# Kernel tuning notes

Measured on AMD Instinct MI355X. Metric: run time of the kernel, lower is better.

The kernel has to match this reference:

```python
import jax, jax.numpy as jnp
import numpy as np

B, S, D, H, DK = 2, 2048, 1024, 16, 64  # d_model = n_heads * d_k

def setup_inputs() -> dict:
    key = jax.random.key(0)
    ks = jax.random.split(key, 11)
    s = 1.0 / np.sqrt(D)
    return {
        "Q": jax.random.normal(ks[0], (B, S, D), jnp.float32),
        "K": jax.random.normal(ks[1], (B, S, D), jnp.float32),
        "V": jax.random.normal(ks[2], (B, S, D), jnp.float32),
        "wq": jax.random.normal(ks[3], (D, D), jnp.float32) * s,
        "bq": jnp.zeros((D,), jnp.float32),
        "wk": jax.random.normal(ks[4], (D, D), jnp.float32) * s,
        "bk": jnp.zeros((D,), jnp.float32),
        "wv": jax.random.normal(ks[5], (D, D), jnp.float32) * s,
        "bv": jnp.zeros((D,), jnp.float32),
        "wo": jax.random.normal(ks[6], (D, D), jnp.float32) * s,
        "bo": jnp.zeros((D,), jnp.float32),
    }

def reference(Q, K, V, wq, bq, wk, bk, wv, bv, wo, bo):
    # linear projections (torch Linear: x @ W^T + b)
    q = Q @ wq.T + bq
    k = K @ wk.T + bk
    v = V @ wv.T + bv
    # split heads -> [B, H, S, DK]
    def split(t):
        return t.reshape(B, S, H, DK).transpose(0, 2, 1, 3)
    q, k, v = split(q), split(k), split(v)
    scale = 1.0 / np.sqrt(DK)
    scores = jnp.einsum('bhqd,bhkd->bhqk', q, k) * scale  # [B,H,S,S]
    probs = jax.nn.softmax(scores, axis=-1)
    # dropout is identity in eval mode
    ctx = jnp.einsum('bhqk,bhkd->bhqd', probs, v)  # [B,H,S,DK]
    ctx = ctx.transpose(0, 2, 1, 3).reshape(B, S, D)
    return ctx @ wo.T + bo
```

## Files before the change

kernel.cpp:

```cpp
#include <hip/hip_runtime.h>

#define S_LEN 2048
#define DMODEL 1024
#define DHEAD 64

typedef _Float16 half8 __attribute__((ext_vector_type(8)));
typedef _Float16 half4 __attribute__((ext_vector_type(4)));
typedef float f32x4 __attribute__((ext_vector_type(4)));
typedef int i32x4 __attribute__((ext_vector_type(4)));

#define LOG2E 1.4426950408889634f

__device__ __forceinline__ void async_copy16(const void* g, void* l) {
  __builtin_amdgcn_global_load_lds((__attribute__((address_space(1))) const void*)g,
                                   (__attribute__((address_space(3))) void*)l,
                                   16, 0, 0);
}

__global__ __launch_bounds__(256) void convert_w(const float* __restrict__ wq,
                                                 const float* __restrict__ wk,
                                                 const float* __restrict__ wv,
                                                 _Float16* __restrict__ dst) {
  const float* src = (blockIdx.y == 0) ? wq : (blockIdx.y == 1) ? wk : wv;
  _Float16* d = dst + (size_t)blockIdx.y * (DMODEL * DMODEL);
  int i = (blockIdx.x * 256 + threadIdx.x) * 4;
  float4 v = *(const float4*)(src + i);
  half4 h;
  h[0] = (_Float16)v.x; h[1] = (_Float16)v.y;
  h[2] = (_Float16)v.z; h[3] = (_Float16)v.w;
  *(half4*)(d + i) = h;
}

__global__ __launch_bounds__(256) void convert_wo(const float* __restrict__ wo,
                                                  _Float16* __restrict__ dst) {
  int i = (blockIdx.x * 256 + threadIdx.x) * 4;
  float4 v = *(const float4*)(wo + i);
  half4 h;
  h[0] = (_Float16)v.x; h[1] = (_Float16)v.y;
  h[2] = (_Float16)v.z; h[3] = (_Float16)v.w;
  *(half4*)(dst + i) = h;
}

__global__ __launch_bounds__(256) void qkv_gemm(
    const float* __restrict__ Qf, const float* __restrict__ Kf, const float* __restrict__ Vf,
    const _Float16* __restrict__ wh,
    const float* __restrict__ bq, const float* __restrict__ bk, const float* __restrict__ bv,
    _Float16* __restrict__ qo, _Float16* __restrict__ ko, _Float16* __restrict__ vt) {
  __shared__ __align__(16) _Float16 As[2][128 * 32];
  __shared__ __align__(16) _Float16 Bs[2][128 * 32];
  const int tid = threadIdx.x;
  const int wave = tid >> 6, lane = tid & 63;
  const int m15 = lane & 15, quad = lane >> 4;
  const int m0 = blockIdx.x * 128;
  const int gn0 = blockIdx.y * 128;
  const int sel = gn0 >> 10;
  const int n0 = gn0 & 1023;
  const float* Ag = (sel == 0) ? Qf : (sel == 1) ? Kf : Vf;
  const _Float16* Wg = wh + (size_t)sel * (DMODEL * DMODEL);
  const float* bias = (sel == 0) ? bq : (sel == 1) ? bk : bv;

  const int wm = (wave & 1) * 64, wn = (wave >> 1) * 64;
  const int sr = tid >> 1, sc16 = (tid & 1) * 16;
  const int g0 = (tid & 1) * 2, asw = (sr >> 1) & 3;
  const int rgr = (quad ^ ((m15 >> 1) & 3)) << 4;

  f32x4 acc[4][4];
#pragma unroll
  for (int i = 0; i < 4; i++)
#pragma unroll
    for (int j = 0; j < 4; j++) {
      f32x4 z = {0.f, 0.f, 0.f, 0.f};
      acc[i][j] = z;
    }

  const float* ap = Ag + (size_t)(m0 + sr) * DMODEL + sc16;
  float4 f0, f1, f2, f3;

  auto issueB = [&](int kk, int nb) {
#pragma unroll
    for (int p = 0; p < 2; p++) {
      int row = p * 64 + (tid >> 2);
      int gl = (tid & 3) ^ ((row >> 1) & 3);
      async_copy16(Wg + (size_t)(n0 + row) * DMODEL + kk + gl * 8,
                   (char*)&Bs[nb][0] + p * 4096 + wave * 1024);
    }
  };
  auto loadA = [&](int kk) {
    const float* p = ap + kk;
    f0 = ((const float4*)p)[0];
    f1 = ((const float4*)p)[1];
    f2 = ((const float4*)p)[2];
    f3 = ((const float4*)p)[3];
  };
  auto writeA = [&](int nb) {
    half8 h0, h1;
    h0[0] = (_Float16)f0.x; h0[1] = (_Float16)f0.y; h0[2] = (_Float16)f0.z; h0[3] = (_Float16)f0.w;
    h0[4] = (_Float16)f1.x; h0[5] = (_Float16)f1.y; h0[6] = (_Float16)f1.z; h0[7] = (_Float16)f1.w;
    h1[0] = (_Float16)f2.x; h1[1] = (_Float16)f2.y; h1[2] = (_Float16)f2.z; h1[3] = (_Float16)f2.w;
    h1[4] = (_Float16)f3.x; h1[5] = (_Float16)f3.y; h1[6] = (_Float16)f3.z; h1[7] = (_Float16)f3.w;
    char* rb = (char*)&As[nb][0] + sr * 64;
    *(half8*)(rb + ((g0 ^ asw) << 4)) = h0;
    *(half8*)(rb + (((g0 + 1) ^ asw) << 4)) = h1;
  };

  issueB(0, 0);
  loadA(0);
  writeA(0);
  __syncthreads();

  for (int kt = 0; kt < 32; kt++) {
    const int buf = kt & 1;
    if (kt < 31) {
      issueB((kt + 1) * 32, buf ^ 1);
      loadA((kt + 1) * 32);
    }
    half8 af[4], bf[4];
#pragma unroll
    for (int i = 0; i < 4; i++)
      af[i] = *(const half8*)((char*)&As[buf][0] + (wm + i * 16 + m15) * 64 + rgr);
#pragma unroll
    for (int j = 0; j < 4; j++)
      bf[j] = *(const half8*)((char*)&Bs[buf][0] + (wn + j * 16 + m15) * 64 + rgr);
#pragma unroll
    for (int i = 0; i < 4; i++)
#pragma unroll
      for (int j = 0; j < 4; j++)
        acc[i][j] = __builtin_amdgcn_mfma_f32_16x16x32_f16(af[i], bf[j], acc[i][j], 0, 0, 0);
    if (kt < 31) writeA(buf ^ 1);
    __syncthreads();
  }
  if (sel != 2) {
    _Float16* outp = (sel == 0) ? qo : ko;
    const float scale = (sel == 0) ? (0.125f * LOG2E) : 1.0f;
#pragma unroll
    for (int i = 0; i < 4; i++) {
#pragma unroll
      for (int j = 0; j < 4; j++) {
        int gn = n0 + wn + j * 16 + m15;
        float bb = bias[gn];
#pragma unroll
        for (int r = 0; r < 4; r++) {
          int gm = m0 + wm + i * 16 + quad * 4 + r;
          outp[(size_t)gm * DMODEL + gn] = (_Float16)((acc[i][j][r] + bb) * scale);
        }
      }
    }
  } else {
#pragma unroll
    for (int i = 0; i < 4; i++) {
      int gm0 = m0 + wm + i * 16 + quad * 4;
      int b = gm0 >> 11, s = gm0 & 2047;
#pragma unroll
      for (int j = 0; j < 4; j++) {
        int gn = n0 + wn + j * 16 + m15;
        int h = gn >> 6, dk = gn & 63;
        float bb = bias[gn];
        half4 hv;
        hv[0] = (_Float16)(acc[i][j][0] + bb);
        hv[1] = (_Float16)(acc[i][j][1] + bb);
        hv[2] = (_Float16)(acc[i][j][2] + bb);
        hv[3] = (_Float16)(acc[i][j][3] + bb);
        *(half4*)(vt + ((size_t)(b * 16 + h) * 64 + dk) * 2048 + s) = hv;
      }
    }
  }
}

__global__ __launch_bounds__(256) void attn_kernel(const _Float16* __restrict__ qh,
                                                   const _Float16* __restrict__ kh,
                                                   const _Float16* __restrict__ vt,
                                                   _Float16* __restrict__ ctx) {
  __shared__ __align__(16) char smem[32768];
  const int tid = threadIdx.x;
  const int wave = tid >> 6, lane = tid & 63;
  const int m15 = lane & 15, qd = lane >> 4;
  const int wq = wave >> 1, ws = wave & 1;
  const int q0 = blockIdx.x * 64;
  const int h = blockIdx.y, b = blockIdx.z;
  const size_t base = (size_t)b * S_LEN * DMODEL + (size_t)h * DHEAD;
  const size_t vbase = (size_t)(b * 16 + h) * 64 * 2048;

  half8 qf[2][2];
#pragma unroll
  for (int qt = 0; qt < 2; qt++) {
    const _Float16* qp = qh + base + (size_t)(q0 + wq * 32 + qt * 16 + m15) * DMODEL + qd * 8;
    qf[qt][0] = *(const half8*)qp;
    qf[qt][1] = *(const half8*)(qp + 32);
  }

  const int l8 = lane >> 3, s8 = lane & 7;
  const int swz = (s8 ^ l8) * 8;
  const _Float16* ksrc = kh + base + (size_t)(wave * 8 + l8) * DMODEL + swz;
  const _Float16* vsrc = vt + vbase + (size_t)(wave * 8 + l8) * S_LEN + swz;
  char* kdst = smem + wave * 1024;
  char* vdst = smem + 16384 + wave * 1024;

  const int kgr = ((qd ^ (m15 & 7)) << 4);
  const int vgr = (((ws * 4 + qd) ^ (m15 & 7)) << 4);
  const int krow = ws * 32 + m15;

  f32x4 acc[4][2];
#pragma unroll
  for (int i = 0; i < 4; i++)
#pragma unroll
    for (int j = 0; j < 2; j++) { f32x4 z = {0.f, 0.f, 0.f, 0.f}; acc[i][j] = z; }
  float ls[2] = {0.f, 0.f};

#pragma unroll
  for (int p = 0; p < 2; p++) {
    async_copy16(ksrc + (size_t)(p * 32) * DMODEL, kdst + p * 4096);
    async_copy16(vsrc + (size_t)(p * 32) * S_LEN, vdst + p * 4096);
  }
  __syncthreads();

  for (int it = 0; it < 32; it++) {
    const int buf = it & 1;
    if (it < 31) {
      const int kv = (it + 1) * 64;
#pragma unroll
      for (int p = 0; p < 2; p++) {
        async_copy16(ksrc + (size_t)(kv + p * 32) * DMODEL, kdst + (buf ^ 1) * 8192 + p * 4096);
        async_copy16(vsrc + (size_t)(p * 32) * S_LEN + kv, vdst + (buf ^ 1) * 8192 + p * 4096);
      }
    }
    const char* kb = smem + buf * 8192;
    const char* vb = smem + 16384 + buf * 8192;

    half8 kf[2][2];
#pragma unroll
    for (int t = 0; t < 2; t++) {
      kf[t][0] = *(const half8*)(kb + (krow + 16 * t) * 128 + kgr);
      kf[t][1] = *(const half8*)(kb + (krow + 16 * t) * 128 + (kgr ^ 64));
    }

    f32x4 sc[2][2];
#pragma unroll
    for (int t = 0; t < 2; t++)
#pragma unroll
      for (int qt = 0; qt < 2; qt++) {
        f32x4 z = {0.f, 0.f, 0.f, 0.f};
        sc[t][qt] = __builtin_amdgcn_mfma_f32_16x16x32_f16(kf[t][0], qf[qt][0], z, 0, 0, 0);
        sc[t][qt] = __builtin_amdgcn_mfma_f32_16x16x32_f16(kf[t][1], qf[qt][1], sc[t][qt], 0, 0, 0);
      }

    int pk[2][2][2];
#pragma unroll
    for (int t = 0; t < 2; t++)
#pragma unroll
      for (int qt = 0; qt < 2; qt++) {
        float e0 = __builtin_amdgcn_exp2f(sc[t][qt][0]);
        float e1 = __builtin_amdgcn_exp2f(sc[t][qt][1]);
        float e2 = __builtin_amdgcn_exp2f(sc[t][qt][2]);
        float e3 = __builtin_amdgcn_exp2f(sc[t][qt][3]);
        ls[qt] += (e0 + e1) + (e2 + e3);
        pk[t][qt][0] = __builtin_bit_cast(int, __builtin_amdgcn_cvt_pkrtz(e0, e1));
        pk[t][qt][1] = __builtin_bit_cast(int, __builtin_amdgcn_cvt_pkrtz(e2, e3));
      }

    half8 pA[2];
#pragma unroll
    for (int qt = 0; qt < 2; qt++) {
      i32x4 fh;
#pragma unroll
      for (int p = 0; p < 2; p++) {
        auto s1 = __builtin_amdgcn_permlane32_swap(pk[0][qt][p], pk[1][qt][p], false, false);
        auto s2 = __builtin_amdgcn_permlane16_swap(s1[0], s1[1], false, false);
        fh[p] = (int)s2[0];
        fh[2 + p] = (int)s2[1];
      }
      pA[qt] = __builtin_bit_cast(half8, fh);
    }

#pragma unroll
    for (int td = 0; td < 4; td++) {
      half8 vf = *(const half8*)(vb + (td * 16 + m15) * 128 + vgr);
#pragma unroll
      for (int qt = 0; qt < 2; qt++)
        acc[td][qt] = __builtin_amdgcn_mfma_f32_16x16x32_f16(vf, pA[qt], acc[td][qt], 0, 0, 0);
    }
    __syncthreads();
  }

  float* Ored = (float*)smem;
  float* Lred = (float*)(smem + 17408);

#pragma unroll
  for (int qt = 0; qt < 2; qt++) {
    ls[qt] += __shfl_xor(ls[qt], 16);
    ls[qt] += __shfl_xor(ls[qt], 32);
  }

  if (ws == 1) {
#pragma unroll
    for (int qt = 0; qt < 2; qt++) {
      int q = wq * 32 + qt * 16 + m15;
      if (qd == 0) Lred[q] = ls[qt];
#pragma unroll
      for (int td = 0; td < 4; td++)
        *(f32x4*)&Ored[q * 68 + td * 16 + qd * 4] = acc[td][qt];
    }
  }
  __syncthreads();

  if (ws == 0) {
#pragma unroll
    for (int qt = 0; qt < 2; qt++) {
      int q = wq * 32 + qt * 16 + m15;
      const float inv = 1.0f / (ls[qt] + Lred[q]);
#pragma unroll
      for (int td = 0; td < 4; td++) {
        f32x4 o = acc[td][qt] + *(const f32x4*)&Ored[q * 68 + td * 16 + qd * 4];
        half4 hv;
#pragma unroll
        for (int r = 0; r < 4; r++) hv[r] = (_Float16)(o[r] * inv);
        *(half4*)(ctx + base + (size_t)(q0 + q) * DMODEL + td * 16 + qd * 4) = hv;
      }
    }
  }
}

__global__ __launch_bounds__(256) void out_gemm(const _Float16* __restrict__ ch,
                                                const _Float16* __restrict__ who,
                                                const float* __restrict__ bo,
                                                float* __restrict__ out) {
  __shared__ __align__(16) _Float16 As[2][64 * 32];
  __shared__ __align__(16) _Float16 Bs[2][128 * 32];
  const int tid = threadIdx.x;
  const int wave = tid >> 6, lane = tid & 63;
  const int m15 = lane & 15, quad = lane >> 4;
  const int m0 = blockIdx.x * 64, n0 = blockIdx.y * 128;
  const int wm = (wave & 1) * 32, wn = (wave >> 1) * 64;
  const int rgr = (quad ^ ((m15 >> 1) & 3)) << 4;

  f32x4 acc[2][4];
#pragma unroll
  for (int i = 0; i < 2; i++)
#pragma unroll
    for (int j = 0; j < 4; j++) {
      f32x4 z = {0.f, 0.f, 0.f, 0.f};
      acc[i][j] = z;
    }

  auto issueAB = [&](int kk, int nb) {
    {
      int row = tid >> 2;
      int gl = (tid & 3) ^ ((row >> 1) & 3);
      async_copy16(ch + (size_t)(m0 + row) * DMODEL + kk + gl * 8,
                   (char*)&As[nb][0] + wave * 1024);
    }
#pragma unroll
    for (int p = 0; p < 2; p++) {
      int row = p * 64 + (tid >> 2);
      int gl = (tid & 3) ^ ((row >> 1) & 3);
      async_copy16(who + (size_t)(n0 + row) * DMODEL + kk + gl * 8,
                   (char*)&Bs[nb][0] + p * 4096 + wave * 1024);
    }
  };

  issueAB(0, 0);
  __syncthreads();

  for (int kt = 0; kt < 32; kt++) {
    const int buf = kt & 1;
    if (kt < 31) issueAB((kt + 1) * 32, buf ^ 1);
    half8 af[2], bf[4];
#pragma unroll
    for (int i = 0; i < 2; i++)
      af[i] = *(const half8*)((char*)&As[buf][0] + (wm + i * 16 + m15) * 64 + rgr);
#pragma unroll
    for (int j = 0; j < 4; j++)
      bf[j] = *(const half8*)((char*)&Bs[buf][0] + (wn + j * 16 + m15) * 64 + rgr);
#pragma unroll
    for (int i = 0; i < 2; i++)
#pragma unroll
      for (int j = 0; j < 4; j++)
        acc[i][j] = __builtin_amdgcn_mfma_f32_16x16x32_f16(af[i], bf[j], acc[i][j], 0, 0, 0);
    __syncthreads();
  }
#pragma unroll
  for (int i = 0; i < 2; i++) {
#pragma unroll
    for (int j = 0; j < 4; j++) {
      int gn = n0 + wn + j * 16 + m15;
      float bb = bo[gn];
#pragma unroll
      for (int r = 0; r < 4; r++) {
        int gm = m0 + wm + i * 16 + quad * 4 + r;
        out[(size_t)gm * DMODEL + gn] = acc[i][j][r] + bb;
      }
    }
  }
}

extern "C" void kernel_launch(void* const* d_in, const int* in_sizes, int n_in,
                              void* d_out, int out_size, void* d_ws, size_t ws_size,
                              hipStream_t stream) {
  (void)in_sizes; (void)n_in; (void)out_size; (void)ws_size;
  const float* Q  = (const float*)d_in[0];
  const float* K  = (const float*)d_in[1];
  const float* V  = (const float*)d_in[2];
  const float* wq = (const float*)d_in[3];
  const float* bq = (const float*)d_in[4];
  const float* wk = (const float*)d_in[5];
  const float* bk = (const float*)d_in[6];
  const float* wv = (const float*)d_in[7];
  const float* bv = (const float*)d_in[8];
  const float* wo = (const float*)d_in[9];
  const float* bo = (const float*)d_in[10];
  float* out = (float*)d_out;

  _Float16* qh = (_Float16*)d_out;
  _Float16* kh = qh + (size_t)4194304;
  _Float16* vt = (_Float16*)d_ws;
  _Float16* wh = vt + (size_t)4194304;
  _Float16* ch = vt + (size_t)4194304;
  _Float16* who = (_Float16*)d_ws;

  convert_w<<<dim3(1024, 3), 256, 0, stream>>>(wq, wk, wv, wh);
  qkv_gemm<<<dim3(32, 24), 256, 0, stream>>>(Q, K, V, wh, bq, bk, bv, qh, kh, vt);
  attn_kernel<<<dim3(32, 16, 2), 256, 0, stream>>>(qh, kh, vt, ch);
  convert_wo<<<dim3(1024), 256, 0, stream>>>(wo, who);
  out_gemm<<<dim3(64, 8), 256, 0, stream>>>(ch, who, bo, out);
}
```

Measured before the change: 272.4 us.

## Stage fp32 activations directly to LDS asynchronously with two-deep prefetch in GEMMs

The QKV GEMM now copies fp32 activation tiles straight into LDS with async global-to-LDS loads and converts them to fp16 at fragment-read time, replacing the register load/convert/store path. Both the QKV and output GEMMs switch to issuing tiles two steps ahead, using explicit vmcnt waits and raw barriers instead of __syncthreads, and add occupancy hints to launch_bounds. This aims to hide global latency and cut register pressure, at the cost of doubling the A-tile LDS footprint and adding per-iteration conversion work and extra barriers.

```diff
diff --git a/kernel.cpp b/kernel.cpp
--- a/kernel.cpp
+++ b/kernel.cpp
@@ -16,6 +16,9 @@
                                    (__attribute__((address_space(3))) void*)l,
                                    16, 0, 0);
 }
+
+#define WAIT_VMCNT(N) asm volatile("s_waitcnt vmcnt(" #N ")" ::: "memory")
+#define RAW_BARRIER() asm volatile("s_barrier" ::: "memory")
 
 __global__ __launch_bounds__(256) void convert_w(const float* __restrict__ wq,
                                                  const float* __restrict__ wk,
@@ -41,12 +44,12 @@
   *(half4*)(dst + i) = h;
 }
 
-__global__ __launch_bounds__(256) void qkv_gemm(
+__global__ __launch_bounds__(256, 3) void qkv_gemm(
     const float* __restrict__ Qf, const float* __restrict__ Kf, const float* __restrict__ Vf,
     const _Float16* __restrict__ wh,
     const float* __restrict__ bq, const float* __restrict__ bk, const float* __restrict__ bv,
     _Float16* __restrict__ qo, _Float16* __restrict__ ko, _Float16* __restrict__ vt) {
-  __shared__ __align__(16) _Float16 As[2][128 * 32];
+  __shared__ __align__(16) float Af[2][128 * 32];
   __shared__ __align__(16) _Float16 Bs[2][128 * 32];
   const int tid = threadIdx.x;
   const int wave = tid >> 6, lane = tid & 63;
@@ -60,9 +63,13 @@
   const float* bias = (sel == 0) ? bq : (sel == 1) ? bk : bv;
 
   const int wm = (wave & 1) * 64, wn = (wave >> 1) * 64;
-  const int sr = tid >> 1, sc16 = (tid & 1) * 16;
-  const int g0 = (tid & 1) * 2, asw = (sr >> 1) & 3;
-  const int rgr = (quad ^ ((m15 >> 1) & 3)) << 4;
+
+  const int a_r = lane >> 3, a_g = (lane & 7) ^ ((lane >> 3) & 7);
+  const int b_r = lane >> 2, b_g = (lane & 3) ^ ((lane >> 3) & 3);
+
+  const int rgrA0 = (((2 * quad) ^ (m15 & 7)) << 4);
+  const int rgrA1 = (((2 * quad + 1) ^ (m15 & 7)) << 4);
+  const int rgrB = ((quad ^ ((m15 >> 1) & 3)) << 4);
 
   f32x4 acc[4][4];
 #pragma unroll
@@ -73,61 +80,60 @@
       acc[i][j] = z;
     }
 
-  const float* ap = Ag + (size_t)(m0 + sr) * DMODEL + sc16;
-  float4 f0, f1, f2, f3;
-
-  auto issueB = [&](int kk, int nb) {
+  auto issueTile = [&](int kk, int nb) {
+#pragma unroll
+    for (int p = 0; p < 4; p++) {
+      int row = (p * 4 + wave) * 8 + a_r;
+      async_copy16(Ag + (size_t)(m0 + row) * DMODEL + kk + a_g * 4,
+                   (char*)&Af[nb][0] + p * 4096 + wave * 1024);
+    }
 #pragma unroll
     for (int p = 0; p < 2; p++) {
-      int row = p * 64 + (tid >> 2);
-      int gl = (tid & 3) ^ ((row >> 1) & 3);
-      async_copy16(Wg + (size_t)(n0 + row) * DMODEL + kk + gl * 8,
+      int row = (p * 4 + wave) * 16 + b_r;
+      async_copy16(Wg + (size_t)(n0 + row) * DMODEL + kk + b_g * 8,
                    (char*)&Bs[nb][0] + p * 4096 + wave * 1024);
     }
   };
-  auto loadA = [&](int kk) {
-    const float* p = ap + kk;
-    f0 = ((const float4*)p)[0];
-    f1 = ((const float4*)p)[1];
-    f2 = ((const float4*)p)[2];
-    f3 = ((const float4*)p)[3];
-  };
-  auto writeA = [&](int nb) {
-    half8 h0, h1;
-    h0[0] = (_Float16)f0.x; h0[1] = (_Float16)f0.y; h0[2] = (_Float16)f0.z; h0[3] = (_Float16)f0.w;
-    h0[4] = (_Float16)f1.x; h0[5] = (_Float16)f1.y; h0[6] = (_Float16)f1.z; h0[7] = (_Float16)f1.w;
-    h1[0] = (_Float16)f2.x; h1[1] = (_Float16)f2.y; h1[2] = (_Float16)f2.z; h1[3] = (_Float16)f2.w;
-    h1[4] = (_Float16)f3.x; h1[5] = (_Float16)f3.y; h1[6] = (_Float16)f3.z; h1[7] = (_Float16)f3.w;
-    char* rb = (char*)&As[nb][0] + sr * 64;
-    *(half8*)(rb + ((g0 ^ asw) << 4)) = h0;
-    *(half8*)(rb + (((g0 + 1) ^ asw) << 4)) = h1;
-  };
-
-  issueB(0, 0);
-  loadA(0);
-  writeA(0);
-  __syncthreads();
+
+  issueTile(0, 0);
+  issueTile(32, 1);
+  WAIT_VMCNT(6);
+  RAW_BARRIER();
 
   for (int kt = 0; kt < 32; kt++) {
     const int buf = kt & 1;
-    if (kt < 31) {
-      issueB((kt + 1) * 32, buf ^ 1);
-      loadA((kt + 1) * 32);
-    }
+    const char* ab = (const char*)&Af[buf][0];
+    const char* bb = (const char*)&Bs[buf][0];
     half8 af[4], bf[4];
 #pragma unroll
-    for (int i = 0; i < 4; i++)
-      af[i] = *(const half8*)((char*)&As[buf][0] + (wm + i * 16 + m15) * 64 + rgr);
+    for (int i = 0; i < 4; i++) {
+      int row = wm + i * 16 + m15;
+      f32x4 lo = *(const f32x4*)(ab + row * 128 + rgrA0);
+      f32x4 hi = *(const f32x4*)(ab + row * 128 + rgrA1);
+      half8 h;
+      h[0] = (_Float16)lo[0]; h[1] = (_Float16)lo[1];
+      h[2] = (_Float16)lo[2]; h[3] = (_Float16)lo[3];
+      h[4] = (_Float16)hi[0]; h[5] = (_Float16)hi[1];
+      h[6] = (_Float16)hi[2]; h[7] = (_Float16)hi[3];
+      af[i] = h;
+    }
 #pragma unroll
     for (int j = 0; j < 4; j++)
-      bf[j] = *(const half8*)((char*)&Bs[buf][0] + (wn + j * 16 + m15) * 64 + rgr);
+      bf[j] = *(const half8*)(bb + (wn + j * 16 + m15) * 64 + rgrB);
 #pragma unroll
     for (int i = 0; i < 4; i++)
 #pragma unroll
       for (int j = 0; j < 4; j++)
         acc[i][j] = __builtin_amdgcn_mfma_f32_16x16x32_f16(af[i], bf[j], acc[i][j], 0, 0, 0);
-    if (kt < 31) writeA(buf ^ 1);
-    __syncthreads();
+    if (kt == 31) break;
+    RAW_BARRIER();
+    if (kt < 30) {
+      issueTile((kt + 2) * 32, buf);
+      WAIT_VMCNT(6);
+    } else {
+      WAIT_VMCNT(0);
+    }
+    RAW_BARRIER();
   }
   if (sel != 2) {
     _Float16* outp = (sel == 0) ? qo : ko;
@@ -319,10 +325,10 @@
   }
 }
 
-__global__ __launch_bounds__(256) void out_gemm(const _Float16* __restrict__ ch,
-                                                const _Float16* __restrict__ who,
-                                                const float* __restrict__ bo,
-                                                float* __restrict__ out) {
+__global__ __launch_bounds__(256, 4) void out_gemm(const _Float16* __restrict__ ch,
+                                                   const _Float16* __restrict__ who,
+                                                   const float* __restrict__ bo,
+                                                   float* __restrict__ out) {
   __shared__ __align__(16) _Float16 As[2][64 * 32];
   __shared__ __align__(16) _Float16 Bs[2][128 * 32];
   const int tid = threadIdx.x;
@@ -330,7 +336,8 @@
   const int m15 = lane & 15, quad = lane >> 4;
   const int m0 = blockIdx.x * 64, n0 = blockIdx.y * 128;
   const int wm = (wave & 1) * 32, wn = (wave >> 1) * 64;
-  const int rgr = (quad ^ ((m15 >> 1) & 3)) << 4;
+  const int b_r = lane >> 2, b_g = (lane & 3) ^ ((lane >> 3) & 3);
+  const int rgr = ((quad ^ ((m15 >> 1) & 3)) << 4);
 
   f32x4 acc[2][4];
 #pragma unroll
@@ -341,28 +348,27 @@
       acc[i][j] = z;
     }
 
-  auto issueAB = [&](int kk, int nb) {
+  auto issueTile = [&](int kk, int nb) {
     {
-      int row = tid >> 2;
-      int gl = (tid & 3) ^ ((row >> 1) & 3);
-      async_copy16(ch + (size_t)(m0 + row) * DMODEL + kk + gl * 8,
+      int row = wave * 16 + b_r;
+      async_copy16(ch + (size_t)(m0 + row) * DMODEL + kk + b_g * 8,
                    (char*)&As[nb][0] + wave * 1024);
     }
 #pragma unroll
     for (int p = 0; p < 2; p++) {
-      int row = p * 64 + (tid >> 2);
-      int gl = (tid & 3) ^ ((row >> 1) & 3);
-      async_copy16(who + (size_t)(n0 + row) * DMODEL + kk + gl * 8,
+      int row = (p * 4 + wave) * 16 + b_r;
+      async_copy16(who + (size_t)(n0 + row) * DMODEL + kk + b_g * 8,
                    (char*)&Bs[nb][0] + p * 4096 + wave * 1024);
     }
   };
 
-  issueAB(0, 0);
-  __syncthreads();
+  issueTile(0, 0);
+  issueTile(32, 1);
+  WAIT_VMCNT(3);
+  RAW_BARRIER();
 
   for (int kt = 0; kt < 32; kt++) {
     const int buf = kt & 1;
-    if (kt < 31) issueAB((kt + 1) * 32, buf ^ 1);
     half8 af[2], bf[4];
 #pragma unroll
     for (int i = 0; i < 2; i++)
@@ -375,7 +381,15 @@
 #pragma unroll
       for (int j = 0; j < 4; j++)
         acc[i][j] = __builtin_amdgcn_mfma_f32_16x16x32_f16(af[i], bf[j], acc[i][j], 0, 0, 0);
-    __syncthreads();
+    if (kt == 31) break;
+    RAW_BARRIER();
+    if (kt < 30) {
+      issueTile((kt + 2) * 32, buf);
+      WAIT_VMCNT(3);
+    } else {
+      WAIT_VMCNT(0);
+    }
+    RAW_BARRIER();
   }
 #pragma unroll
   for (int i = 0; i < 2; i++) {
```

Result: faster. 236.9 us (-13.0%).

## Deepen async LDS prefetch pipelines with explicit vmcnt waits across all kernels

Applied to the files above, without the earlier changes.

Reworks the load pipelines of the QKV GEMM, attention and output GEMM kernels. Tiles are now prefetched two steps ahead: triple-buffered B and K/V tiles, and a two-deep issue in out_gemm. The __syncthreads calls are replaced with targeted s_waitcnt vmcnt/lgkmcnt plus raw s_barrier, so loads stay in flight across iterations and global latency is hidden better. This costs more LDS (48KB in attention) and adds occupancy hints. Correctness now depends on the hand-counted vmcnt values.

```diff
diff --git a/kernel.cpp b/kernel.cpp
--- a/kernel.cpp
+++ b/kernel.cpp
@@ -16,6 +16,10 @@
                                    (__attribute__((address_space(3))) void*)l,
                                    16, 0, 0);
 }
+
+#define WAIT_VMCNT(N) asm volatile("s_waitcnt vmcnt(" #N ")" ::: "memory")
+#define WAIT_LGKM0() asm volatile("s_waitcnt lgkmcnt(0)" ::: "memory")
+#define RAW_BARRIER() asm volatile("s_barrier" ::: "memory")
 
 __global__ __launch_bounds__(256) void convert_w(const float* __restrict__ wq,
                                                  const float* __restrict__ wk,
@@ -41,13 +45,13 @@
   *(half4*)(dst + i) = h;
 }
 
-__global__ __launch_bounds__(256) void qkv_gemm(
+__global__ __launch_bounds__(256, 3) void qkv_gemm(
     const float* __restrict__ Qf, const float* __restrict__ Kf, const float* __restrict__ Vf,
     const _Float16* __restrict__ wh,
     const float* __restrict__ bq, const float* __restrict__ bk, const float* __restrict__ bv,
     _Float16* __restrict__ qo, _Float16* __restrict__ ko, _Float16* __restrict__ vt) {
-  __shared__ __align__(16) _Float16 As[2][128 * 32];
-  __shared__ __align__(16) _Float16 Bs[2][128 * 32];
+  __shared__ __align__(16) _Float16 Asb[2][128 * 32];
+  __shared__ __align__(16) _Float16 Bsb[3][128 * 32];
   const int tid = threadIdx.x;
   const int wave = tid >> 6, lane = tid & 63;
   const int m15 = lane & 15, quad = lane >> 4;
@@ -60,9 +64,11 @@
   const float* bias = (sel == 0) ? bq : (sel == 1) ? bk : bv;
 
   const int wm = (wave & 1) * 64, wn = (wave >> 1) * 64;
+
   const int sr = tid >> 1, sc16 = (tid & 1) * 16;
   const int g0 = (tid & 1) * 2, asw = (sr >> 1) & 3;
-  const int rgr = (quad ^ ((m15 >> 1) & 3)) << 4;
+  const int b_r = lane >> 2, b_g = (lane & 3) ^ ((lane >> 3) & 3);
+  const int ra = ((quad ^ ((m15 >> 1) & 3)) << 4);
 
   f32x4 acc[4][4];
 #pragma unroll
@@ -76,15 +82,6 @@
   const float* ap = Ag + (size_t)(m0 + sr) * DMODEL + sc16;
   float4 f0, f1, f2, f3;
 
-  auto issueB = [&](int kk, int nb) {
-#pragma unroll
-    for (int p = 0; p < 2; p++) {
-      int row = p * 64 + (tid >> 2);
-      int gl = (tid & 3) ^ ((row >> 1) & 3);
-      async_copy16(Wg + (size_t)(n0 + row) * DMODEL + kk + gl * 8,
-                   (char*)&Bs[nb][0] + p * 4096 + wave * 1024);
-    }
-  };
   auto loadA = [&](int kk) {
     const float* p = ap + kk;
     f0 = ((const float4*)p)[0];
@@ -98,36 +95,56 @@
     h0[4] = (_Float16)f1.x; h0[5] = (_Float16)f1.y; h0[6] = (_Float16)f1.z; h0[7] = (_Float16)f1.w;
     h1[0] = (_Float16)f2.x; h1[1] = (_Float16)f2.y; h1[2] = (_Float16)f2.z; h1[3] = (_Float16)f2.w;
     h1[4] = (_Float16)f3.x; h1[5] = (_Float16)f3.y; h1[6] = (_Float16)f3.z; h1[7] = (_Float16)f3.w;
-    char* rb = (char*)&As[nb][0] + sr * 64;
+    char* rb = (char*)&Asb[nb][0] + sr * 64;
     *(half8*)(rb + ((g0 ^ asw) << 4)) = h0;
     *(half8*)(rb + (((g0 + 1) ^ asw) << 4)) = h1;
   };
-
+  auto issueB = [&](int kk, int nb) {
+#pragma unroll
+    for (int p = 0; p < 2; p++) {
+      int row = (p * 4 + wave) * 16 + b_r;
+      async_copy16(Wg + (size_t)(n0 + row) * DMODEL + kk + b_g * 8,
+                   (char*)&Bsb[nb][0] + p * 4096 + wave * 1024);
+    }
+  };
+
+  loadA(0);
   issueB(0, 0);
-  loadA(0);
+  issueB(32, 1);
+  WAIT_VMCNT(4);
   writeA(0);
-  __syncthreads();
-
+  WAIT_VMCNT(2);
+  WAIT_LGKM0();
+  RAW_BARRIER();
+
+  int bcur = 0, bnxt = 2;
   for (int kt = 0; kt < 32; kt++) {
-    const int buf = kt & 1;
-    if (kt < 31) {
-      issueB((kt + 1) * 32, buf ^ 1);
-      loadA((kt + 1) * 32);
-    }
+    const int bufA = kt & 1;
+    if (kt < 31) loadA((kt + 1) * 32);
+    if (kt < 30) issueB((kt + 2) * 32, bnxt);
+
+    const char* ab = (const char*)&Asb[bufA][0];
+    const char* bb = (const char*)&Bsb[bcur][0];
     half8 af[4], bf[4];
 #pragma unroll
     for (int i = 0; i < 4; i++)
-      af[i] = *(const half8*)((char*)&As[buf][0] + (wm + i * 16 + m15) * 64 + rgr);
+      af[i] = *(const half8*)(ab + (wm + i * 16 + m15) * 64 + ra);
 #pragma unroll
     for (int j = 0; j < 4; j++)
-      bf[j] = *(const half8*)((char*)&Bs[buf][0] + (wn + j * 16 + m15) * 64 + rgr);
+      bf[j] = *(const half8*)(bb + (wn + j * 16 + m15) * 64 + ra);
 #pragma unroll
     for (int i = 0; i < 4; i++)
 #pragma unroll
       for (int j = 0; j < 4; j++)
         acc[i][j] = __builtin_amdgcn_mfma_f32_16x16x32_f16(af[i], bf[j], acc[i][j], 0, 0, 0);
-    if (kt < 31) writeA(buf ^ 1);
-    __syncthreads();
+
+    if (kt == 31) break;
+    if (kt < 30) { WAIT_VMCNT(2); } else { WAIT_VMCNT(0); }
+    writeA(bufA ^ 1);
+    WAIT_LGKM0();
+    RAW_BARRIER();
+    bcur = (bcur == 2) ? 0 : bcur + 1;
+    bnxt = (bnxt == 2) ? 0 : bnxt + 1;
   }
   if (sel != 2) {
     _Float16* outp = (sel == 0) ? qo : ko;
@@ -170,7 +187,7 @@
                                                    const _Float16* __restrict__ kh,
                                                    const _Float16* __restrict__ vt,
                                                    _Float16* __restrict__ ctx) {
-  __shared__ __align__(16) char smem[32768];
+  __shared__ __align__(16) char smem[49152];
   const int tid = threadIdx.x;
   const int wave = tid >> 6, lane = tid & 63;
   const int m15 = lane & 15, qd = lane >> 4;
@@ -192,13 +209,22 @@
   const int swz = (s8 ^ l8) * 8;
   const _Float16* ksrc = kh + base + (size_t)(wave * 8 + l8) * DMODEL + swz;
   const _Float16* vsrc = vt + vbase + (size_t)(wave * 8 + l8) * S_LEN + swz;
-  char* kdst = smem + wave * 1024;
-  char* vdst = smem + 16384 + wave * 1024;
 
   const int kgr = ((qd ^ (m15 & 7)) << 4);
   const int vgr = (((ws * 4 + qd) ^ (m15 & 7)) << 4);
   const int krow = ws * 32 + m15;
 
+  auto stage = [&](int tile, int bufi) {
+    const int kv = tile * 64;
+    char* kd = smem + bufi * 8192 + wave * 1024;
+    char* vd = smem + 24576 + bufi * 8192 + wave * 1024;
+#pragma unroll
+    for (int p = 0; p < 2; p++) {
+      async_copy16(ksrc + (size_t)(kv + p * 32) * DMODEL, kd + p * 4096);
+      async_copy16(vsrc + (size_t)(p * 32) * S_LEN + kv, vd + p * 4096);
+    }
+  };
+
   f32x4 acc[4][2];
 #pragma unroll
   for (int i = 0; i < 4; i++)
@@ -206,25 +232,16 @@
     for (int j = 0; j < 2; j++) { f32x4 z = {0.f, 0.f, 0.f, 0.f}; acc[i][j] = z; }
   float ls[2] = {0.f, 0.f};
 
-#pragma unroll
-  for (int p = 0; p < 2; p++) {
-    async_copy16(ksrc + (size_t)(p * 32) * DMODEL, kdst + p * 4096);
-    async_copy16(vsrc + (size_t)(p * 32) * S_LEN, vdst + p * 4096);
-  }
-  __syncthreads();
-
+  stage(0, 0);
+  stage(1, 1);
+  WAIT_VMCNT(4);
+  RAW_BARRIER();
+
+  int bcur = 0, bnxt = 2;
   for (int it = 0; it < 32; it++) {
-    const int buf = it & 1;
-    if (it < 31) {
-      const int kv = (it + 1) * 64;
-#pragma unroll
-      for (int p = 0; p < 2; p++) {
-        async_copy16(ksrc + (size_t)(kv + p * 32) * DMODEL, kdst + (buf ^ 1) * 8192 + p * 4096);
-        async_copy16(vsrc + (size_t)(p * 32) * S_LEN + kv, vdst + (buf ^ 1) * 8192 + p * 4096);
-      }
-    }
-    const char* kb = smem + buf * 8192;
-    const char* vb = smem + 16384 + buf * 8192;
+    if (it < 30) stage(it + 2, bnxt);
+    const char* kb = smem + bcur * 8192;
+    const char* vb = smem + 24576 + bcur * 8192;
 
     half8 kf[2][2];
 #pragma unroll
@@ -278,7 +295,10 @@
       for (int qt = 0; qt < 2; qt++)
         acc[td][qt] = __builtin_amdgcn_mfma_f32_16x16x32_f16(vf, pA[qt], acc[td][qt], 0, 0, 0);
     }
-    __syncthreads();
+    if (it < 30) { WAIT_VMCNT(4); } else { WAIT_VMCNT(0); }
+    RAW_BARRIER();
+    bcur = (bcur == 2) ? 0 : bcur + 1;
+    bnxt = (bnxt == 2) ? 0 : bnxt + 1;
   }
 
   float* Ored = (float*)smem;
@@ -319,10 +339,10 @@
   }
 }
 
-__global__ __launch_bounds__(256) void out_gemm(const _Float16* __restrict__ ch,
-                                                const _Float16* __restrict__ who,
-                                                const float* __restrict__ bo,
-                                                float* __restrict__ out) {
+__global__ __launch_bounds__(256, 4) void out_gemm(const _Float16* __restrict__ ch,
+                                                   const _Float16* __restrict__ who,
+                                                   const float* __restrict__ bo,
+                                                   float* __restrict__ out) {
   __shared__ __align__(16) _Float16 As[2][64 * 32];
   __shared__ __align__(16) _Float16 Bs[2][128 * 32];
   const int tid = threadIdx.x;
@@ -330,7 +350,8 @@
   const int m15 = lane & 15, quad = lane >> 4;
   const int m0 = blockIdx.x * 64, n0 = blockIdx.y * 128;
   const int wm = (wave & 1) * 32, wn = (wave >> 1) * 64;
-  const int rgr = (quad ^ ((m15 >> 1) & 3)) << 4;
+  const int b_r = lane >> 2, b_g = (lane & 3) ^ ((lane >> 3) & 3);
+  const int rgr = ((quad ^ ((m15 >> 1) & 3)) << 4);
 
   f32x4 acc[2][4];
 #pragma unroll
@@ -341,28 +362,27 @@
       acc[i][j] = z;
     }
 
-  auto issueAB = [&](int kk, int nb) {
+  auto issueTile = [&](int kk, int nb) {
     {
-      int row = tid >> 2;
-      int gl = (tid & 3) ^ ((row >> 1) & 3);
-      async_copy16(ch + (size_t)(m0 + row) * DMODEL + kk + gl * 8,
+      int row = wave * 16 + b_r;
+      async_copy16(ch + (size_t)(m0 + row) * DMODEL + kk + b_g * 8,
                    (char*)&As[nb][0] + wave * 1024);
     }
 #pragma unroll
     for (int p = 0; p < 2; p++) {
-      int row = p * 64 + (tid >> 2);
-      int gl = (tid & 3) ^ ((row >> 1) & 3);
-      async_copy16(who + (size_t)(n0 + row) * DMODEL + kk + gl * 8,
+      int row = (p * 4 + wave) * 16 + b_r;
+      async_copy16(who + (size_t)(n0 + row) * DMODEL + kk + b_g * 8,
                    (char*)&Bs[nb][0] + p * 4096 + wave * 1024);
     }
   };
 
-  issueAB(0, 0);
-  __syncthreads();
+  issueTile(0, 0);
+  issueTile(32, 1);
+  WAIT_VMCNT(3);
+  RAW_BARRIER();
 
   for (int kt = 0; kt < 32; kt++) {
     const int buf = kt & 1;
-    if (kt < 31) issueAB((kt + 1) * 32, buf ^ 1);
     half8 af[2], bf[4];
 #pragma unroll
     for (int i = 0; i < 2; i++)
@@ -375,7 +395,15 @@
 #pragma unroll
       for (int j = 0; j < 4; j++)
         acc[i][j] = __builtin_amdgcn_mfma_f32_16x16x32_f16(af[i], bf[j], acc[i][j], 0, 0, 0);
-    __syncthreads();
+    if (kt == 31) break;
+    RAW_BARRIER();
+    if (kt < 30) {
+      issueTile((kt + 2) * 32, buf);
+      WAIT_VMCNT(3);
+    } else {
+      WAIT_VMCNT(0);
+    }
+    RAW_BARRIER();
   }
 #pragma unroll
   for (int i = 0; i < 2; i++) {
```

Result: faster. 239.2 us (-12.2%).
